# Kernel tuning notes

Hardware: AMD Instinct MI355X
Metric: run time of the kernel (lower is better)

## Reference

```python
import jax, jax.numpy as jnp
import numpy as np

N_NODES = 50000
N_EDGES = 300000
D = 256
N_RELS = 500


def setup_inputs() -> dict:
    key = jax.random.key(0)
    ks = jax.random.split(key, 12)
    s = 1.0 / np.sqrt(D)  # keep activations O(1) through the dense transforms
    return {
        "h": jax.random.normal(ks[0], (N_NODES, D), dtype=jnp.float32),
        "prev_h": jax.random.normal(ks[1], (N_NODES, D), dtype=jnp.float32),
        "emb_rel": jax.random.normal(ks[2], (N_RELS, D), dtype=jnp.float32),
        "norm": jax.random.uniform(ks[3], (N_NODES, 1), dtype=jnp.float32),
        "weight_neighbor": jax.random.normal(ks[4], (D, D), dtype=jnp.float32) * s,
        "loop_weight": jax.random.normal(ks[5], (D, D), dtype=jnp.float32) * s,
        "evolve_loop_weight": jax.random.normal(ks[6], (D, D), dtype=jnp.float32) * s,
        "skip_connect_weight": jax.random.normal(ks[7], (D, D), dtype=jnp.float32) * s,
        "skip_connect_bias": jnp.zeros((D,), dtype=jnp.float32),
        "src": jax.random.randint(ks[8], (N_EDGES,), 0, N_NODES),
        "dst": jax.random.randint(ks[9], (N_EDGES,), 0, N_NODES),
        "etype": jax.random.randint(ks[10], (N_EDGES,), 0, N_RELS),
    }


def reference(h, prev_h, emb_rel, norm, weight_neighbor, loop_weight,
              evolve_loop_weight, skip_connect_weight, skip_connect_bias,
              src, dst, etype):
    n_nodes = h.shape[0]
    # msg_func: per-edge gather of src features + relation embedding, dense transform
    msg = (h[src] + emb_rel[etype]) @ weight_neighbor          # [E, D]
    # fn.sum: segment-sum messages into destination nodes
    agg = jax.ops.segment_sum(msg, dst, num_segments=n_nodes)  # [N, D]
    # apply_func: multiply by per-node norm
    agg = agg * norm
    # self-loop: loop_weight where in_degree > 0, evolve_loop_weight otherwise
    in_deg = jax.ops.segment_sum(jnp.ones_like(dst), dst, num_segments=n_nodes)
    has_in = (in_deg > 0)[:, None]
    loop_message = jnp.where(has_in, h @ loop_weight, h @ evolve_loop_weight)
    # skip connection gate
    skip_weight = jax.nn.sigmoid(prev_h @ skip_connect_weight + skip_connect_bias)
    node_repr = skip_weight * (agg + loop_message) + (1.0 - skip_weight) * prev_h
    return jax.nn.relu(node_repr)
```

## Files before the change

### kernel.cpp

```cpp
#include <hip/hip_runtime.h>
#include <cstdint>
#include <cstddef>

#define N_NODES 50000
#define N_EDGES 300000
#define DIM     256
#define KTOT    768
#define N_RELS  500

#define SCAN_BLK  256
#define SCAN_NBLK ((N_NODES + SCAN_BLK - 1) / SCAN_BLK)

#define CONV_ELEMS ((N_NODES + N_RELS) * DIM)
#define CONV_BLKS  ((CONV_ELEMS / 8 + 255) / 256)
#define WT_BLKS    48
#define HIST_BLKS  ((N_EDGES + 255) / 256)

typedef unsigned short u16;
typedef __attribute__((ext_vector_type(8))) short short8v;
typedef __attribute__((ext_vector_type(4))) float float4v;

static __device__ __forceinline__ u16 f2bf(float f) {
    union { float f; unsigned u; } v; v.f = f;
    unsigned u = v.u;
    unsigned r = u + 0x7FFFu + ((u >> 16) & 1u);
    return (u16)(r >> 16);
}
static __device__ __forceinline__ float bf2f(u16 b) {
    union { unsigned u; float f; } v; v.u = ((unsigned)b) << 16; return v.f;
}

static __device__ __forceinline__ void gld16(const void* g, u16* l) {
    __builtin_amdgcn_global_load_lds(
        (const __attribute__((address_space(1))) unsigned int*)g,
        (__attribute__((address_space(3))) unsigned int*)l,
        16, 0, 0);
}

static __device__ __forceinline__ void acc8(float* a, uint4 hv, uint4 ev) {
    const unsigned* hw = (const unsigned*)&hv;
    const unsigned* ew = (const unsigned*)&ev;
#pragma unroll
    for (int j = 0; j < 4; j++) {
        a[2*j]   += bf2f((u16)(hw[j] & 0xffffu)) + bf2f((u16)(ew[j] & 0xffffu));
        a[2*j+1] += bf2f((u16)(hw[j] >> 16))     + bf2f((u16)(ew[j] >> 16));
    }
}

__global__ void prep_kernel(const float* __restrict__ h, const float* __restrict__ emb,
                            const float* __restrict__ Wn, const float* __restrict__ Wl,
                            const float* __restrict__ Wsc, const int* __restrict__ dstv,
                            u16* __restrict__ Xh, u16* __restrict__ embb,
                            u16* __restrict__ Wt, int* __restrict__ deg) {
    __shared__ float T[64][65];
    int b = blockIdx.x;
    if (b < CONV_BLKS) {
        int i = b * 256 + threadIdx.x;
        int e0 = i * 8;
        if (e0 >= CONV_ELEMS) return;
        const float* s; u16* d;
        if (e0 < N_NODES * DIM) { s = h + e0; d = Xh + e0; }
        else { int o = e0 - N_NODES * DIM; s = emb + o; d = embb + o; }
        float4 a = *(const float4*)(s);
        float4 c2 = *(const float4*)(s + 4);
        u16 o8[8] = { f2bf(a.x), f2bf(a.y), f2bf(a.z), f2bf(a.w),
                      f2bf(c2.x), f2bf(c2.y), f2bf(c2.z), f2bf(c2.w) };
        *(uint4*)d = *(const uint4*)o8;
    } else if (b < CONV_BLKS + WT_BLKS) {
        int tb  = b - CONV_BLKS;
        int mat = tb >> 4;
        int kb  = (tb & 15) >> 2;
        int db  = tb & 3;
        const float* W = (mat == 0) ? Wn : ((mat == 1) ? Wl : Wsc);
        int c  = threadIdx.x & 63;
        int rq = threadIdx.x >> 6;
#pragma unroll
        for (int p = 0; p < 16; p++) {
            int kk = rq + p * 4;
            T[kk][c] = W[(kb * 64 + kk) * DIM + db * 64 + c];
        }
        __syncthreads();
#pragma unroll
        for (int p = 0; p < 16; p++) {
            int dd = rq + p * 4;
            Wt[(size_t)(db * 64 + dd) * KTOT + mat * 256 + kb * 64 + c] = f2bf(T[c][dd]);
        }
    } else {
        int e = (b - CONV_BLKS - WT_BLKS) * 256 + threadIdx.x;
        if (e < N_EDGES) atomicAdd(&deg[dstv[e]], 1);
    }
}

__global__ void scanA_kernel(const int* __restrict__ deg, int* __restrict__ excl_local,
                             int* __restrict__ block_sum) {
    __shared__ int sdata[SCAN_BLK];
    int t = threadIdx.x, i = blockIdx.x * SCAN_BLK + t;
    int v = (i < N_NODES) ? deg[i] : 0;
    sdata[t] = v;
    __syncthreads();
    for (int off = 1; off < SCAN_BLK; off <<= 1) {
        int u = (t >= off) ? sdata[t - off] : 0;
        __syncthreads();
        sdata[t] += u;
        __syncthreads();
    }
    if (i < N_NODES) excl_local[i] = sdata[t] - v;
    if (t == SCAN_BLK - 1) block_sum[blockIdx.x] = sdata[t];
}

__global__ void scanB_kernel(const int* __restrict__ block_sum, int* __restrict__ block_base,
                             int* __restrict__ offsets) {
    __shared__ int sdata[SCAN_NBLK];
    int t = threadIdx.x;
    int v = (t < SCAN_NBLK) ? block_sum[t] : 0;
    if (t < SCAN_NBLK) sdata[t] = v;
    __syncthreads();
    for (int off = 1; off < SCAN_NBLK; off <<= 1) {
        int u = (t >= off && t < SCAN_NBLK) ? sdata[t - off] : 0;
        __syncthreads();
        if (t < SCAN_NBLK) sdata[t] += u;
        __syncthreads();
    }
    if (t < SCAN_NBLK) block_base[t] = sdata[t] - v;
    if (t == SCAN_NBLK - 1) offsets[N_NODES] = sdata[t];
}

__global__ void scanC_kernel(const int* __restrict__ excl_local, const int* __restrict__ block_base,
                             int* __restrict__ offsets, int* __restrict__ cursor) {
    int i = blockIdx.x * SCAN_BLK + threadIdx.x;
    if (i < N_NODES) {
        int e = block_base[blockIdx.x] + excl_local[i];
        offsets[i] = e; cursor[i] = e;
    }
}

__global__ void scatter_kernel(const int* __restrict__ src, const int* __restrict__ dstv,
                               const int* __restrict__ et, int* __restrict__ cursor,
                               unsigned* __restrict__ esee) {
    int e = blockIdx.x * 256 + threadIdx.x;
    if (e >= N_EDGES) return;
    int d = dstv[e];
    int pos = atomicAdd(&cursor[d], 1);
    esee[pos] = (unsigned)src[e] * N_RELS + (unsigned)et[e];
}

__global__ void agg_kernel(const u16* __restrict__ Xh, const u16* __restrict__ embb,
                           const float* __restrict__ norm, const int* __restrict__ offsets,
                           const unsigned* __restrict__ esee, const float* __restrict__ prev_h,
                           u16* __restrict__ Xa, u16* __restrict__ Xp,
                           int* __restrict__ wl_count, int* __restrict__ wl) {
    int wave = (blockIdx.x * 256 + threadIdx.x) >> 6;
    int half = (threadIdx.x >> 5) & 1;
    int lane32 = threadIdx.x & 31;
    int n = wave * 2 + half;
    if (n >= N_NODES) return;
    int s0 = offsets[n], s1 = offsets[n + 1];
    int c8 = lane32 * 8;
    float4 pa = *(const float4*)(prev_h + (size_t)n * DIM + c8);
    float4 pb = *(const float4*)(prev_h + (size_t)n * DIM + c8 + 4);
    float acc[8] = {0.f, 0.f, 0.f, 0.f, 0.f, 0.f, 0.f, 0.f};
    int e = s0;
    for (; e + 3 < s1; e += 4) {
        unsigned v0 = esee[e], v1 = esee[e + 1], v2 = esee[e + 2], v3 = esee[e + 3];
        unsigned sa = v0 / N_RELS, ta = v0 - sa * N_RELS;
        unsigned sb = v1 / N_RELS, tb = v1 - sb * N_RELS;
        unsigned sc = v2 / N_RELS, tc = v2 - sc * N_RELS;
        unsigned sd = v3 / N_RELS, td = v3 - sd * N_RELS;
        uint4 ha = *(const uint4*)(Xh + (size_t)sa * DIM + c8);
        uint4 ea = *(const uint4*)(embb + (size_t)ta * DIM + c8);
        uint4 hb = *(const uint4*)(Xh + (size_t)sb * DIM + c8);
        uint4 eb = *(const uint4*)(embb + (size_t)tb * DIM + c8);
        uint4 hc = *(const uint4*)(Xh + (size_t)sc * DIM + c8);
        uint4 ec = *(const uint4*)(embb + (size_t)tc * DIM + c8);
        uint4 hd = *(const uint4*)(Xh + (size_t)sd * DIM + c8);
        uint4 ed = *(const uint4*)(embb + (size_t)td * DIM + c8);
        acc8(acc, ha, ea); acc8(acc, hb, eb); acc8(acc, hc, ec); acc8(acc, hd, ed);
    }
    for (; e < s1; e++) {
        unsigned v = esee[e];
        unsigned s = v / N_RELS;
        unsigned t = v - s * N_RELS;
        uint4 hv = *(const uint4*)(Xh + (size_t)s * DIM + c8);
        uint4 ev = *(const uint4*)(embb + (size_t)t * DIM + c8);
        acc8(acc, hv, ev);
    }
    float nr = norm[n];
    u16 o[8];
#pragma unroll
    for (int j = 0; j < 8; j++) o[j] = f2bf(acc[j] * nr);
    *(uint4*)(Xa + (size_t)n * DIM + c8) = *(const uint4*)o;
    u16 p8[8] = { f2bf(pa.x), f2bf(pa.y), f2bf(pa.z), f2bf(pa.w),
                  f2bf(pb.x), f2bf(pb.y), f2bf(pb.z), f2bf(pb.w) };
    *(uint4*)(Xp + (size_t)n * DIM + c8) = *(const uint4*)p8;
    if (lane32 == 0 && s1 == s0) { int idx = atomicAdd(wl_count, 1); wl[idx] = n; }
}

__launch_bounds__(512, 4)
__global__ void gemm_kernel(const u16* __restrict__ Xa, const u16* __restrict__ Xh,
                            const u16* __restrict__ Xp, const u16* __restrict__ Wt,
                            const float* __restrict__ prev_h, const float* __restrict__ bias,
                            float* __restrict__ out) {
    __shared__ __align__(16) u16 lds[40960];
    int tid  = threadIdx.x;
    int wave = tid >> 6, lane = tid & 63, q = lane >> 4, m16 = lane & 15;
    int wm = wave >> 2;
    int wnn = (wave & 3) * 64;
    int m0 = blockIdx.x * 64;
    int lr = lane >> 3, lc8 = lane & 7;
    int sc8 = (lc8 ^ lr) << 3;

    int arow = wave * 8 + lr;
    int ga = (m0 + arow < N_NODES) ? (m0 + arow) : (N_NODES - 1);
    const u16* sAa = Xa + (size_t)ga * DIM + sc8;
    const u16* sAh = Xh + (size_t)ga * DIM + sc8;
    const u16* sAp = Xp + (size_t)ga * DIM + sc8;
    const u16* sB = Wt + (size_t)(wave * 32 + lr) * KTOT + sc8;

    float4v acc1[2][4], acc2[2][4];
#pragma unroll
    for (int i = 0; i < 2; i++)
#pragma unroll
        for (int j = 0; j < 4; j++) { acc1[i][j] = (float4v)0.f; acc2[i][j] = (float4v)0.f; }

    auto stage = [&](int kt, int buf) {
#pragma unroll
        for (int j = 0; j < 4; j++)
            gld16(sB + (size_t)j * 8 * KTOT + kt * 64,
                  &lds[8192 + buf * 16384 + wave * 2048 + j * 512]);
        const u16* base = (kt < 4) ? sAa : ((kt < 8) ? sAh : sAp);
        gld16(base + (kt & 3) * 64, &lds[buf * 4096 + wave * 512]);
    };

    stage(0, 0);
    stage(1, 1);

    int sw = (m16 & 7) << 3;

#pragma unroll
    for (int kt = 0; kt < 12; kt++) {
        int buf = kt & 1;
        if (kt < 11) asm volatile("s_waitcnt vmcnt(5)" ::: "memory");
        else         asm volatile("s_waitcnt vmcnt(0)" ::: "memory");
        __builtin_amdgcn_sched_barrier(0);
        __builtin_amdgcn_s_barrier();
        __builtin_amdgcn_sched_barrier(0);

#pragma unroll
        for (int kk = 0; kk < 2; kk++) {
            int ck = (kk * 32 + q * 8) ^ sw;
            short8v af[2], bfr[4];
#pragma unroll
            for (int mi = 0; mi < 2; mi++)
                af[mi] = *(const short8v*)(&lds[buf * 4096 + (wm * 32 + mi * 16 + m16) * 64 + ck]);
#pragma unroll
            for (int ni = 0; ni < 4; ni++)
                bfr[ni] = *(const short8v*)(&lds[8192 + buf * 16384 + (wnn + ni * 16 + m16) * 64 + ck]);
            if (kt < 8) {
#pragma unroll
                for (int mi = 0; mi < 2; mi++)
#pragma unroll
                    for (int ni = 0; ni < 4; ni++)
                        acc1[mi][ni] = __builtin_amdgcn_mfma_f32_16x16x32_bf16(
                            af[mi], bfr[ni], acc1[mi][ni], 0, 0, 0);
            } else {
#pragma unroll
                for (int mi = 0; mi < 2; mi++)
#pragma unroll
                    for (int ni = 0; ni < 4; ni++)
                        acc2[mi][ni] = __builtin_amdgcn_mfma_f32_16x16x32_bf16(
                            af[mi], bfr[ni], acc2[mi][ni], 0, 0, 0);
            }
        }

        __builtin_amdgcn_sched_barrier(0);
        __builtin_amdgcn_s_barrier();
        __builtin_amdgcn_sched_barrier(0);
        if (kt + 2 < 12) stage(kt + 2, buf);
    }

#pragma unroll
    for (int mi = 0; mi < 2; mi++) {
#pragma unroll
        for (int ni = 0; ni < 4; ni++) {
            int d = wnn + ni * 16 + m16;
            float b = bias[d];
#pragma unroll
            for (int r = 0; r < 4; r++) {
                int node = m0 + wm * 32 + mi * 16 + q * 4 + r;
                if (node < N_NODES) {
                    float S  = acc2[mi][ni][r] + b;
                    float sg = 1.f / (1.f + __expf(-S));
                    float ph = prev_h[(size_t)node * DIM + d];
                    float v  = sg * acc1[mi][ni][r] + (1.f - sg) * ph;
                    out[(size_t)node * DIM + d] = fmaxf(v, 0.f);
                }
            }
        }
    }
}

__global__ void fixup_kernel(const float* __restrict__ h, const float* __restrict__ prev_h,
                             const float* __restrict__ We, const float* __restrict__ Wsc,
                             const float* __restrict__ bias, const int* __restrict__ wl_count,
                             const int* __restrict__ wl, float* __restrict__ out) {
    __shared__ float ph[DIM], hh[DIM];
    int d = threadIdx.x;
    int cnt = *wl_count;
    for (int i = blockIdx.x; i < cnt; i += gridDim.x) {
        int n = wl[i];
        ph[d] = prev_h[(size_t)n * DIM + d];
        hh[d] = h[(size_t)n * DIM + d];
        __syncthreads();
        float s = 0.f, l = 0.f;
        for (int k = 0; k < DIM; k++) {
            s += ph[k] * Wsc[k * DIM + d];
            l += hh[k] * We[k * DIM + d];
        }
        float sg = 1.f / (1.f + __expf(-(s + bias[d])));
        float v = sg * l + (1.f - sg) * ph[d];
        out[(size_t)n * DIM + d] = fmaxf(v, 0.f);
        __syncthreads();
    }
}

extern "C" void kernel_launch(void* const* d_in, const int* in_sizes, int n_in,
                              void* d_out, int out_size, void* d_ws, size_t ws_size,
                              hipStream_t stream) {
    const float* h      = (const float*)d_in[0];
    const float* prev_h = (const float*)d_in[1];
    const float* emb    = (const float*)d_in[2];
    const float* norm   = (const float*)d_in[3];
    const float* Wn     = (const float*)d_in[4];
    const float* Wl     = (const float*)d_in[5];
    const float* We     = (const float*)d_in[6];
    const float* Wsc    = (const float*)d_in[7];
    const float* bias   = (const float*)d_in[8];
    const int*   src    = (const int*)d_in[9];
    const int*   dstv   = (const int*)d_in[10];
    const int*   et     = (const int*)d_in[11];
    float* out = (float*)d_out;

    char* ws = (char*)d_ws;
    size_t off = 0;
    auto alloc = [&](size_t bytes) -> char* {
        char* p = ws + off; off += (bytes + 255) & ~(size_t)255; return p;
    };
    u16* Xa      = (u16*)alloc((size_t)N_NODES * DIM * 2);
    u16* Xh      = (u16*)alloc((size_t)N_NODES * DIM * 2);
    u16* Xp      = (u16*)alloc((size_t)N_NODES * DIM * 2);
    u16* embb    = (u16*)alloc((size_t)N_RELS * DIM * 2);
    u16* Wt      = (u16*)alloc((size_t)DIM * KTOT * 2);
    int* deg     = (int*)alloc((size_t)N_NODES * 4);
    int* wlcnt   = (int*)alloc(16);
    int* wl      = (int*)alloc((size_t)N_NODES * 4);
    int* offsets = (int*)alloc((size_t)(N_NODES + 1) * 4);
    int* cursor  = (int*)alloc((size_t)N_NODES * 4);
    unsigned* esee = (unsigned*)alloc((size_t)N_EDGES * 4);
    int* excl    = (int*)alloc((size_t)N_NODES * 4);
    int* bsum    = (int*)alloc((size_t)SCAN_NBLK * 4);
    int* bbase   = (int*)alloc((size_t)SCAN_NBLK * 4);

    hipMemsetAsync(deg, 0, (size_t)N_NODES * 4, stream);
    hipMemsetAsync(wlcnt, 0, 4, stream);

    prep_kernel<<<CONV_BLKS + WT_BLKS + HIST_BLKS, 256, 0, stream>>>(
        h, emb, Wn, Wl, Wsc, dstv, Xh, embb, Wt, deg);
    scanA_kernel<<<SCAN_NBLK, SCAN_BLK, 0, stream>>>(deg, excl, bsum);
    scanB_kernel<<<1, SCAN_BLK, 0, stream>>>(bsum, bbase, offsets);
    scanC_kernel<<<SCAN_NBLK, SCAN_BLK, 0, stream>>>(excl, bbase, offsets, cursor);
    scatter_kernel<<<(N_EDGES + 255) / 256, 256, 0, stream>>>(src, dstv, et, cursor, esee);
    agg_kernel<<<(N_NODES / 2 + 3) / 4, 256, 0, stream>>>(Xh, embb, norm, offsets, esee, prev_h,
                                                          Xa, Xp, wlcnt, wl);
    gemm_kernel<<<(N_NODES + 63) / 64, 512, 0, stream>>>(Xa, Xh, Xp, Wt, prev_h, bias, out);
    fixup_kernel<<<256, 256, 0, stream>>>(h, prev_h, We, Wsc, bias, wlcnt, wl, out);
}
```

Measured before the change: 311.7 us.

## Merge CSR-build prep, scan and scatter kernels into one cooperative kernel

Replaces the two memsets and five small launches (prep, three scan phases, scatter) with a single cooperative kernel of 1024 blocks that separates the phases with grid-wide syncs. The aim is to remove per-launch overhead and inter-kernel gaps on the serial CSR-construction chain. In exchange, work becomes grid-strided over a fixed block count, and each grid.sync adds a device-wide barrier. The kernel relies on 1024 blocks of 256 threads being co-resident for the cooperative launch to succeed.

```diff
diff --git a/kernel.cpp b/kernel.cpp
--- a/kernel.cpp
+++ b/kernel.cpp
@@ -1,6 +1,9 @@
 #include <hip/hip_runtime.h>
+#include <hip/hip_cooperative_groups.h>
 #include <cstdint>
 #include <cstddef>
+
+namespace cg = cooperative_groups;
 
 #define N_NODES 50000
 #define N_EDGES 300000
@@ -8,13 +11,11 @@
 #define KTOT    768
 #define N_RELS  500
 
-#define SCAN_BLK  256
-#define SCAN_NBLK ((N_NODES + SCAN_BLK - 1) / SCAN_BLK)
+#define SCAN_NBLK ((N_NODES + 255) / 256)
+#define WT_BLKS   48
+#define COOP_BLKS 1024
 
 #define CONV_ELEMS ((N_NODES + N_RELS) * DIM)
-#define CONV_BLKS  ((CONV_ELEMS / 8 + 255) / 256)
-#define WT_BLKS    48
-#define HIST_BLKS  ((N_EDGES + 255) / 256)
 
 typedef unsigned short u16;
 typedef __attribute__((ext_vector_type(8))) short short8v;
@@ -47,17 +48,29 @@
     }
 }
 
-__global__ void prep_kernel(const float* __restrict__ h, const float* __restrict__ emb,
-                            const float* __restrict__ Wn, const float* __restrict__ Wl,
-                            const float* __restrict__ Wsc, const int* __restrict__ dstv,
-                            u16* __restrict__ Xh, u16* __restrict__ embb,
-                            u16* __restrict__ Wt, int* __restrict__ deg) {
+__global__ void __launch_bounds__(256, 4)
+csr_kernel(const float* __restrict__ h, const float* __restrict__ emb,
+           const float* __restrict__ Wn, const float* __restrict__ Wl,
+           const float* __restrict__ Wsc,
+           const int* __restrict__ src, const int* __restrict__ dstv,
+           const int* __restrict__ et,
+           u16* __restrict__ Xh, u16* __restrict__ embb, u16* __restrict__ Wt,
+           int* __restrict__ deg, int* __restrict__ wlcnt,
+           int* __restrict__ excl, int* __restrict__ bsum, int* __restrict__ bbase,
+           int* __restrict__ offsets, int* __restrict__ cursor,
+           unsigned* __restrict__ esee) {
+    cg::grid_group grid = cg::this_grid();
     __shared__ float T[64][65];
-    int b = blockIdx.x;
-    if (b < CONV_BLKS) {
-        int i = b * 256 + threadIdx.x;
+    __shared__ int   sdata[256];
+    int t = threadIdx.x;
+    int gtid = blockIdx.x * 256 + t;
+    const int gsz = COOP_BLKS * 256;
+
+    for (int i = gtid; i < N_NODES; i += gsz) deg[i] = 0;
+    if (gtid == 0) wlcnt[0] = 0;
+
+    for (int i = gtid; i < CONV_ELEMS / 8; i += gsz) {
         int e0 = i * 8;
-        if (e0 >= CONV_ELEMS) return;
         const float* s; u16* d;
         if (e0 < N_NODES * DIM) { s = h + e0; d = Xh + e0; }
         else { int o = e0 - N_NODES * DIM; s = emb + o; d = embb + o; }
@@ -66,14 +79,16 @@
         u16 o8[8] = { f2bf(a.x), f2bf(a.y), f2bf(a.z), f2bf(a.w),
                       f2bf(c2.x), f2bf(c2.y), f2bf(c2.z), f2bf(c2.w) };
         *(uint4*)d = *(const uint4*)o8;
-    } else if (b < CONV_BLKS + WT_BLKS) {
-        int tb  = b - CONV_BLKS;
+    }
+
+    if (blockIdx.x < WT_BLKS) {
+        int tb  = blockIdx.x;
         int mat = tb >> 4;
         int kb  = (tb & 15) >> 2;
         int db  = tb & 3;
         const float* W = (mat == 0) ? Wn : ((mat == 1) ? Wl : Wsc);
-        int c  = threadIdx.x & 63;
-        int rq = threadIdx.x >> 6;
+        int c  = t & 63;
+        int rq = t >> 6;
 #pragma unroll
         for (int p = 0; p < 16; p++) {
             int kk = rq + p * 4;
@@ -85,63 +100,54 @@
             int dd = rq + p * 4;
             Wt[(size_t)(db * 64 + dd) * KTOT + mat * 256 + kb * 64 + c] = f2bf(T[c][dd]);
         }
-    } else {
-        int e = (b - CONV_BLKS - WT_BLKS) * 256 + threadIdx.x;
-        if (e < N_EDGES) atomicAdd(&deg[dstv[e]], 1);
-    }
-}
-
-__global__ void scanA_kernel(const int* __restrict__ deg, int* __restrict__ excl_local,
-                             int* __restrict__ block_sum) {
-    __shared__ int sdata[SCAN_BLK];
-    int t = threadIdx.x, i = blockIdx.x * SCAN_BLK + t;
-    int v = (i < N_NODES) ? deg[i] : 0;
-    sdata[t] = v;
-    __syncthreads();
-    for (int off = 1; off < SCAN_BLK; off <<= 1) {
-        int u = (t >= off) ? sdata[t - off] : 0;
-        __syncthreads();
-        sdata[t] += u;
-        __syncthreads();
-    }
-    if (i < N_NODES) excl_local[i] = sdata[t] - v;
-    if (t == SCAN_BLK - 1) block_sum[blockIdx.x] = sdata[t];
-}
-
-__global__ void scanB_kernel(const int* __restrict__ block_sum, int* __restrict__ block_base,
-                             int* __restrict__ offsets) {
-    __shared__ int sdata[SCAN_NBLK];
-    int t = threadIdx.x;
-    int v = (t < SCAN_NBLK) ? block_sum[t] : 0;
-    if (t < SCAN_NBLK) sdata[t] = v;
-    __syncthreads();
-    for (int off = 1; off < SCAN_NBLK; off <<= 1) {
-        int u = (t >= off && t < SCAN_NBLK) ? sdata[t - off] : 0;
-        __syncthreads();
-        if (t < SCAN_NBLK) sdata[t] += u;
-        __syncthreads();
-    }
-    if (t < SCAN_NBLK) block_base[t] = sdata[t] - v;
-    if (t == SCAN_NBLK - 1) offsets[N_NODES] = sdata[t];
-}
-
-__global__ void scanC_kernel(const int* __restrict__ excl_local, const int* __restrict__ block_base,
-                             int* __restrict__ offsets, int* __restrict__ cursor) {
-    int i = blockIdx.x * SCAN_BLK + threadIdx.x;
-    if (i < N_NODES) {
-        int e = block_base[blockIdx.x] + excl_local[i];
+    }
+    grid.sync();
+
+    for (int e = gtid; e < N_EDGES; e += gsz) atomicAdd(&deg[dstv[e]], 1);
+    grid.sync();
+
+    if (blockIdx.x < SCAN_NBLK) {
+        int i = blockIdx.x * 256 + t;
+        int v = (i < N_NODES) ? deg[i] : 0;
+        sdata[t] = v;
+        __syncthreads();
+        for (int off = 1; off < 256; off <<= 1) {
+            int u = (t >= off) ? sdata[t - off] : 0;
+            __syncthreads();
+            sdata[t] += u;
+            __syncthreads();
+        }
+        if (i < N_NODES) excl[i] = sdata[t] - v;
+        if (t == 255) bsum[blockIdx.x] = sdata[t];
+    }
+    grid.sync();
+
+    if (blockIdx.x == 0) {
+        int v = (t < SCAN_NBLK) ? bsum[t] : 0;
+        sdata[t] = v;
+        __syncthreads();
+        for (int off = 1; off < 256; off <<= 1) {
+            int u = (t >= off) ? sdata[t - off] : 0;
+            __syncthreads();
+            sdata[t] += u;
+            __syncthreads();
+        }
+        if (t < SCAN_NBLK) bbase[t] = sdata[t] - v;
+        if (t == SCAN_NBLK - 1) offsets[N_NODES] = sdata[t];
+    }
+    grid.sync();
+
+    for (int i = gtid; i < N_NODES; i += gsz) {
+        int e = bbase[i >> 8] + excl[i];
         offsets[i] = e; cursor[i] = e;
     }
-}
-
-__global__ void scatter_kernel(const int* __restrict__ src, const int* __restrict__ dstv,
-                               const int* __restrict__ et, int* __restrict__ cursor,
-                               unsigned* __restrict__ esee) {
-    int e = blockIdx.x * 256 + threadIdx.x;
-    if (e >= N_EDGES) return;
-    int d = dstv[e];
-    int pos = atomicAdd(&cursor[d], 1);
-    esee[pos] = (unsigned)src[e] * N_RELS + (unsigned)et[e];
+    grid.sync();
+
+    for (int e = gtid; e < N_EDGES; e += gsz) {
+        int d = dstv[e];
+        int pos = atomicAdd(&cursor[d], 1);
+        esee[pos] = (unsigned)src[e] * N_RELS + (unsigned)et[e];
+    }
 }
 
 __global__ void agg_kernel(const u16* __restrict__ Xh, const u16* __restrict__ embb,
@@ -360,15 +366,14 @@
     int* bsum    = (int*)alloc((size_t)SCAN_NBLK * 4);
     int* bbase   = (int*)alloc((size_t)SCAN_NBLK * 4);
 
-    hipMemsetAsync(deg, 0, (size_t)N_NODES * 4, stream);
-    hipMemsetAsync(wlcnt, 0, 4, stream);
-
-    prep_kernel<<<CONV_BLKS + WT_BLKS + HIST_BLKS, 256, 0, stream>>>(
-        h, emb, Wn, Wl, Wsc, dstv, Xh, embb, Wt, deg);
-    scanA_kernel<<<SCAN_NBLK, SCAN_BLK, 0, stream>>>(deg, excl, bsum);
-    scanB_kernel<<<1, SCAN_BLK, 0, stream>>>(bsum, bbase, offsets);
-    scanC_kernel<<<SCAN_NBLK, SCAN_BLK, 0, stream>>>(excl, bbase, offsets, cursor);
-    scatter_kernel<<<(N_EDGES + 255) / 256, 256, 0, stream>>>(src, dstv, et, cursor, esee);
+    void* args[] = { (void*)&h, (void*)&emb, (void*)&Wn, (void*)&Wl, (void*)&Wsc,
+                     (void*)&src, (void*)&dstv, (void*)&et,
+                     (void*)&Xh, (void*)&embb, (void*)&Wt, (void*)&deg, (void*)&wlcnt,
+                     (void*)&excl, (void*)&bsum, (void*)&bbase,
+                     (void*)&offsets, (void*)&cursor, (void*)&esee };
+    hipLaunchCooperativeKernel((const void*)csr_kernel, dim3(COOP_BLKS), dim3(256),
+                               args, 0, stream);
+
     agg_kernel<<<(N_NODES / 2 + 3) / 4, 256, 0, stream>>>(Xh, embb, norm, offsets, esee, prev_h,
                                                           Xa, Xp, wlcnt, wl);
     gemm_kernel<<<(N_NODES + 63) / 64, 512, 0, stream>>>(Xa, Xh, Xp, Wt, prev_h, bias, out);
```

Result: slower. 871.5 us (+179.6%).
